# Optimization experiments

Measured on AMD Instinct MI355X. Metric: run time of the kernel, lower is better.

## Reference

```python
import jax, jax.numpy as jnp
import numpy as np

B, IN, H = 4096, 512, 1024
ALPHA, RHO = 0.001, 0.05

def setup_inputs() -> dict:
    key = jax.random.key(0)
    ks = jax.random.split(key, 9)
    inp = jax.random.normal(ks[0], (B, IN), dtype=jnp.float32)
    time = jax.random.uniform(ks[1], (B, 1), dtype=jnp.float32) * 100.0
    hx = jax.random.normal(ks[2], (B, H), dtype=jnp.float32)
    cx = jax.random.normal(ks[3], (B, H), dtype=jnp.float32)
    # params (match torch init scales loosely)
    Wxh_w = jax.random.normal(ks[4], (4 * H, IN), dtype=jnp.float32) / np.sqrt(IN)
    Wxh_b = jnp.zeros((4 * H,), dtype=jnp.float32)
    Whh_w = jax.random.normal(ks[5], (4 * H, H), dtype=jnp.float32) / np.sqrt(H)
    tau = jax.random.normal(ks[6], (H,), dtype=jnp.float32) * 0.5 + 5.0
    s = jax.random.uniform(ks[7], (H,), dtype=jnp.float32) * tau
    alpha = jnp.array([ALPHA], dtype=jnp.float32)
    rho = jnp.array([RHO], dtype=jnp.float32)
    return {"input": inp, "time": time, "hx": hx, "cx": cx,
            "Wxh_w": Wxh_w, "Wxh_b": Wxh_b, "Whh_w": Whh_w,
            "tau": tau, "s": s, "alpha": alpha, "rho": rho}

def _time_gate(time, s, tau, alpha, rho):
    # phi: [B, H] (time [B,1] broadcast against s/tau [H])
    phi = jnp.fmod(time - s, tau) / tau
    k = jnp.where(phi < rho / 2.0, 2.0 * phi / rho,
        jnp.where(phi < rho, 2.0 - 2.0 * phi / rho, alpha * phi))
    # computed under torch.no_grad() in the original
    return jax.lax.stop_gradient(k)

def reference(input, time, hx, cx, Wxh_w, Wxh_b, Whh_w, tau, s, alpha, rho):
    gates = input @ Wxh_w.T + Wxh_b + hx @ Whh_w.T  # [B, 4H]
    i, f, g, o = jnp.split(gates, 4, axis=1)
    k = _time_gate(time, s, tau, alpha, rho)
    ft = jax.nn.sigmoid(f + 1.0 - k)
    it = jax.nn.sigmoid(i) * k
    gt = jnp.tanh(g) * k
    ot = jax.nn.sigmoid(o) * k
    cy = ft * cx + it * gt
    hy = ot * jnp.tanh(cy)
    return (hy, cy)
```

## Files before the change

kernel.cpp:

```cpp
#include <hip/hip_runtime.h>

#define AS1 __attribute__((address_space(1)))
#define AS3 __attribute__((address_space(3)))

typedef _Float16 half_t;
typedef __attribute__((ext_vector_type(8))) _Float16 f16x8;
typedef __attribute__((ext_vector_type(4))) float f32x4;

static constexpr int Bsz = 4096;
static constexpr int INs = 512;
static constexpr int Hs  = 1024;
static constexpr int BM  = 128;
static constexpr int BH  = 32;
static constexpr int BK  = 64;
static constexpr int NIT = INs / BK + Hs / BK;

static constexpr size_t XN  = (size_t)Bsz * INs;
static constexpr size_t HXN = (size_t)Bsz * Hs;
static constexpr size_t WXN = (size_t)4 * Hs * INs;
static constexpr size_t WHN = (size_t)4 * Hs * Hs;
static constexpr size_t OFF_X  = 0;
static constexpr size_t OFF_HX = XN;
static constexpr size_t OFF_WX = XN + HXN;
static constexpr size_t OFF_WH = XN + HXN + WXN;
static constexpr size_t TOT    = XN + HXN + WXN + WHN;
static constexpr size_t KN     = (size_t)Bsz * Hs;

__device__ __forceinline__ float sigm(float x) {
  return 1.0f / (1.0f + __expf(-x));
}
__device__ __forceinline__ float tanh_fast(float x) {
  const float e = __expf(2.0f * x);
  return 1.0f - 2.0f / (e + 1.0f);
}

__global__ __launch_bounds__(256)
void cvt_kernel(const float* __restrict__ x, const float* __restrict__ hx,
                const float* __restrict__ wx, const float* __restrict__ wh,
                const float* __restrict__ timep, const float* __restrict__ sp,
                const float* __restrict__ taup, const float* __restrict__ alphap,
                const float* __restrict__ rhop,
                half_t* __restrict__ ws, float* __restrict__ kout) {
  const size_t cid = (size_t)blockIdx.x * 256 + threadIdx.x;
  if (cid < TOT / 8) {
    const size_t e = cid * 8;
    const float* src; size_t off;
    if (e < OFF_HX)      { src = x;  off = e - OFF_X; }
    else if (e < OFF_WX) { src = hx; off = e - OFF_HX; }
    else if (e < OFF_WH) { src = wx; off = e - OFF_WX; }
    else                 { src = wh; off = e - OFF_WH; }
    const f32x4 a = *(const f32x4*)(src + off);
    const f32x4 b = *(const f32x4*)(src + off + 4);
    f16x8 o;
    o[0]=(half_t)a[0]; o[1]=(half_t)a[1]; o[2]=(half_t)a[2]; o[3]=(half_t)a[3];
    o[4]=(half_t)b[0]; o[5]=(half_t)b[1]; o[6]=(half_t)b[2]; o[7]=(half_t)b[3];
    *(f16x8*)(ws + e) = o;
  } else {
    const size_t e2 = (cid - TOT / 8) * 8;
    const int b = (int)(e2 >> 10);
    const int h = (int)(e2 & 1023);
    const float tv = timep[b];
    const float alphav = alphap[0];
    const float rhov   = rhop[0];
    const float rh     = 0.5f * rhov;
    const f32x4 s0 = *(const f32x4*)(sp + h),   s1 = *(const f32x4*)(sp + h + 4);
    const f32x4 t0 = *(const f32x4*)(taup + h), t1 = *(const f32x4*)(taup + h + 4);
    f32x4 k0, k1;
    #pragma unroll
    for (int j = 0; j < 8; ++j) {
      const float sv   = j < 4 ? s0[j] : s1[j - 4];
      const float tauv = j < 4 ? t0[j] : t1[j - 4];
      const float phi = fmodf(tv - sv, tauv) / tauv;
      float kv;
      if (phi < rh)        kv = (2.0f * phi) / rhov;
      else if (phi < rhov) kv = 2.0f - (2.0f * phi) / rhov;
      else                 kv = alphav * phi;
      if (j < 4) k0[j] = kv; else k1[j - 4] = kv;
    }
    *(f32x4*)(kout + e2) = k0;
    *(f32x4*)(kout + e2 + 4) = k1;
  }
}

__global__ __launch_bounds__(256, 4)
void plstm_gemm(const half_t* __restrict__ xin,
                const half_t* __restrict__ hxp,
                const float* __restrict__ cxp,
                const half_t* __restrict__ wxh,
                const float* __restrict__ biasp,
                const half_t* __restrict__ whh,
                const float* __restrict__ kp,
                float* __restrict__ outp)
{
  __shared__ half_t As[BM * BK];
  __shared__ half_t Bs[BM * BK];

  const int tid  = threadIdx.x;
  const int w    = tid >> 6;
  const int lane = tid & 63;
  const int l15  = lane & 15;
  const int grp  = lane >> 4;
  const int wr   = w >> 1;
  const int wc   = w & 1;

  const int m0 = blockIdx.x * BM;
  const int h0 = blockIdx.y * BH;

  f32x4 acc[4][4] = {};

  const int ldr = tid >> 3;
  const int ldc = tid & 7;

  for (int it = 0; it < NIT; ++it) {
    const bool p1 = it >= INs / BK;
    const half_t* Ap = p1 ? hxp : xin;
    const half_t* Wp = p1 ? whh : wxh;
    const int Ka = p1 ? Hs : INs;
    const int k0 = (p1 ? (it - INs / BK) : it) * BK;
    #pragma unroll
    for (int i = 0; i < 4; ++i) {
      const int e    = i * 32 + ldr;
      const int gc8  = ldc ^ (e & 7);
      const int wrow = ((e >> 4) & 3) * Hs + h0 + ((e >> 6) << 4) + (e & 15);
      const half_t* ga = Ap + (size_t)(m0 + e) * Ka + (k0 + gc8 * 8);
      __builtin_amdgcn_global_load_lds((AS1 void*)ga,
                                       (AS3 void*)(As + (e * 8 + ldc) * 8), 16, 0, 0);
      const half_t* gw = Wp + (size_t)wrow * Ka + (k0 + gc8 * 8);
      __builtin_amdgcn_global_load_lds((AS1 void*)gw,
                                       (AS3 void*)(Bs + (e * 8 + ldc) * 8), 16, 0, 0);
    }
    __syncthreads();

    #pragma unroll
    for (int kk = 0; kk < 2; ++kk) {
      const int c8x = kk * 4 + grp;
      f16x8 af[4], bfr[4];
      #pragma unroll
      for (int mt = 0; mt < 4; ++mt) {
        const int e = wr * 64 + mt * 16 + l15;
        af[mt] = *(const f16x8*)(As + (e * 8 + (c8x ^ (l15 & 7))) * 8);
      }
      #pragma unroll
      for (int nt = 0; nt < 4; ++nt) {
        const int e = wc * 64 + nt * 16 + l15;
        bfr[nt] = *(const f16x8*)(Bs + (e * 8 + (c8x ^ (l15 & 7))) * 8);
      }
      #pragma unroll
      for (int mt = 0; mt < 4; ++mt)
        #pragma unroll
        for (int nt = 0; nt < 4; ++nt)
          acc[mt][nt] = __builtin_amdgcn_mfma_f32_16x16x32_f16(
              af[mt], bfr[nt], acc[mt][nt], 0, 0, 0);
    }
    __syncthreads();
  }

  const int h = h0 + wc * 16 + l15;
  const float bi  = biasp[h];
  const float bfv = biasp[Hs + h];
  const float bg  = biasp[2 * Hs + h];
  const float bo  = biasp[3 * Hs + h];

  #pragma unroll
  for (int mt = 0; mt < 4; ++mt) {
    #pragma unroll
    for (int r = 0; r < 4; ++r) {
      const int brow = m0 + wr * 64 + mt * 16 + grp * 4 + r;
      const float kv = kp[(size_t)brow * Hs + h];
      const float iv = acc[mt][0][r] + bi;
      const float fv = acc[mt][1][r] + bfv;
      const float gv = acc[mt][2][r] + bg;
      const float ov = acc[mt][3][r] + bo;

      const float cxv = cxp[(size_t)brow * Hs + h];
      const float ft = sigm(fv + 1.0f - kv);
      const float it2 = sigm(iv) * kv;
      const float gt = tanh_fast(gv) * kv;
      const float ot = sigm(ov) * kv;
      const float cy = ft * cxv + it2 * gt;
      const float hy = ot * tanh_fast(cy);

      outp[(size_t)brow * Hs + h] = hy;
      outp[(size_t)Bsz * Hs + (size_t)brow * Hs + h] = cy;
    }
  }
}

__global__ __launch_bounds__(256, 3)
void plstm_gemm_f32(const float* __restrict__ xin, const float* __restrict__ timep,
                    const float* __restrict__ hxp, const float* __restrict__ cxp,
                    const float* __restrict__ wxh, const float* __restrict__ biasp,
                    const float* __restrict__ whh, const float* __restrict__ taup,
                    const float* __restrict__ sp, const float* __restrict__ alphap,
                    const float* __restrict__ rhop, float* __restrict__ outp)
{
  __shared__ half_t As[BM * BK];
  __shared__ half_t Bs[BM * BK];

  const int tid  = threadIdx.x;
  const int w    = tid >> 6;
  const int lane = tid & 63;
  const int l15  = lane & 15;
  const int grp  = lane >> 4;
  const int wr   = w >> 1;
  const int wc   = w & 1;

  const int m0 = blockIdx.x * BM;
  const int h0 = blockIdx.y * BH;

  f32x4 acc[4][4] = {};
  const int ldr = tid >> 3;
  const int ldc = tid & 7;

  for (int it = 0; it < NIT; ++it) {
    const bool p1 = it >= INs / BK;
    const float* Ap = p1 ? hxp : xin;
    const float* Wp = p1 ? whh : wxh;
    const int Ka = p1 ? Hs : INs;
    const int k0 = (p1 ? (it - INs / BK) : it) * BK;
    #pragma unroll
    for (int i = 0; i < 4; ++i) {
      const int e    = i * 32 + ldr;
      const int gc8  = ldc ^ (e & 7);
      const int wrow = ((e >> 4) & 3) * Hs + h0 + ((e >> 6) << 4) + (e & 15);
      const float* ga = Ap + (size_t)(m0 + e) * Ka + (k0 + gc8 * 8);
      const f32x4 a0 = *(const f32x4*)ga, a1 = *(const f32x4*)(ga + 4);
      f16x8 pa;
      pa[0]=(half_t)a0[0]; pa[1]=(half_t)a0[1]; pa[2]=(half_t)a0[2]; pa[3]=(half_t)a0[3];
      pa[4]=(half_t)a1[0]; pa[5]=(half_t)a1[1]; pa[6]=(half_t)a1[2]; pa[7]=(half_t)a1[3];
      *(f16x8*)(As + (e * 8 + ldc) * 8) = pa;
      const float* gw = Wp + (size_t)wrow * Ka + (k0 + gc8 * 8);
      const f32x4 b0 = *(const f32x4*)gw, b1 = *(const f32x4*)(gw + 4);
      f16x8 pb;
      pb[0]=(half_t)b0[0]; pb[1]=(half_t)b0[1]; pb[2]=(half_t)b0[2]; pb[3]=(half_t)b0[3];
      pb[4]=(half_t)b1[0]; pb[5]=(half_t)b1[1]; pb[6]=(half_t)b1[2]; pb[7]=(half_t)b1[3];
      *(f16x8*)(Bs + (e * 8 + ldc) * 8) = pb;
    }
    __syncthreads();
    #pragma unroll
    for (int kk = 0; kk < 2; ++kk) {
      const int c8x = kk * 4 + grp;
      f16x8 af[4], bfr[4];
      #pragma unroll
      for (int mt = 0; mt < 4; ++mt) {
        const int e = wr * 64 + mt * 16 + l15;
        af[mt] = *(const f16x8*)(As + (e * 8 + (c8x ^ (l15 & 7))) * 8);
      }
      #pragma unroll
      for (int nt = 0; nt < 4; ++nt) {
        const int e = wc * 64 + nt * 16 + l15;
        bfr[nt] = *(const f16x8*)(Bs + (e * 8 + (c8x ^ (l15 & 7))) * 8);
      }
      #pragma unroll
      for (int mt = 0; mt < 4; ++mt)
        #pragma unroll
        for (int nt = 0; nt < 4; ++nt)
          acc[mt][nt] = __builtin_amdgcn_mfma_f32_16x16x32_f16(
              af[mt], bfr[nt], acc[mt][nt], 0, 0, 0);
    }
    __syncthreads();
  }

  const int h = h0 + wc * 16 + l15;
  const float bi  = biasp[h];
  const float bfv = biasp[Hs + h];
  const float bg  = biasp[2 * Hs + h];
  const float bo  = biasp[3 * Hs + h];
  const float sv = sp[h], tauv = taup[h];
  const float alphav = alphap[0], rhov = rhop[0], rh = 0.5f * rhov;

  #pragma unroll
  for (int mt = 0; mt < 4; ++mt) {
    #pragma unroll
    for (int r = 0; r < 4; ++r) {
      const int brow = m0 + wr * 64 + mt * 16 + grp * 4 + r;
      const float tv = timep[brow];
      const float phi = fmodf(tv - sv, tauv) / tauv;
      float kv;
      if (phi < rh)        kv = (2.0f * phi) / rhov;
      else if (phi < rhov) kv = 2.0f - (2.0f * phi) / rhov;
      else                 kv = alphav * phi;
      const float iv = acc[mt][0][r] + bi;
      const float fv = acc[mt][1][r] + bfv;
      const float gv = acc[mt][2][r] + bg;
      const float ov = acc[mt][3][r] + bo;
      const float cxv = cxp[(size_t)brow * Hs + h];
      const float ft = sigm(fv + 1.0f - kv);
      const float it2 = sigm(iv) * kv;
      const float gt = tanh_fast(gv) * kv;
      const float ot = sigm(ov) * kv;
      const float cy = ft * cxv + it2 * gt;
      const float hy = ot * tanh_fast(cy);
      outp[(size_t)brow * Hs + h] = hy;
      outp[(size_t)Bsz * Hs + (size_t)brow * Hs + h] = cy;
    }
  }
}

extern "C" void kernel_launch(void* const* d_in, const int* in_sizes, int n_in,
                              void* d_out, int out_size, void* d_ws, size_t ws_size,
                              hipStream_t stream) {
  (void)in_sizes; (void)n_in; (void)out_size;
  const float* xin   = (const float*)d_in[0];
  const float* timep = (const float*)d_in[1];
  const float* hxp   = (const float*)d_in[2];
  const float* cxp   = (const float*)d_in[3];
  const float* wxh   = (const float*)d_in[4];
  const float* biasp = (const float*)d_in[5];
  const float* whh   = (const float*)d_in[6];
  const float* taup  = (const float*)d_in[7];
  const float* sp    = (const float*)d_in[8];
  const float* alphap= (const float*)d_in[9];
  const float* rhop  = (const float*)d_in[10];
  float* outp = (float*)d_out;

  dim3 grid(Bsz / BM, Hs / BH);
  const bool wsK = ws_size >= TOT * sizeof(half_t) + KN * sizeof(float);

  if (wsK) {
    half_t* ws = (half_t*)d_ws;
    float* kout = (float*)(ws + TOT);
    const int nchunk = (int)(TOT / 8 + KN / 8);
    cvt_kernel<<<nchunk / 256, 256, 0, stream>>>(xin, hxp, wxh, whh,
                                                 timep, sp, taup, alphap, rhop,
                                                 ws, kout);
    plstm_gemm<<<grid, 256, 0, stream>>>(
        ws + OFF_X, ws + OFF_HX, cxp, ws + OFF_WX, biasp, ws + OFF_WH,
        kout, outp);
  } else {
    plstm_gemm_f32<<<grid, 256, 0, stream>>>(
        xin, timep, hxp, cxp, wxh, biasp, whh,
        taup, sp, alphap, rhop, outp);
  }
}
```

Measured before the change: 198.5 us.

## Fuse time gate into GEMM epilogue, double-buffer A tile, load weights directly

```diff
diff --git a/kernel.cpp b/kernel.cpp
--- a/kernel.cpp
+++ b/kernel.cpp
@@ -24,7 +24,6 @@
 static constexpr size_t OFF_WX = XN + HXN;
 static constexpr size_t OFF_WH = XN + HXN + WXN;
 static constexpr size_t TOT    = XN + HXN + WXN + WHN;
-static constexpr size_t KN     = (size_t)Bsz * Hs;
 
 __device__ __forceinline__ float sigm(float x) {
   return 1.0f / (1.0f + __expf(-x));
@@ -37,49 +36,20 @@
 __global__ __launch_bounds__(256)
 void cvt_kernel(const float* __restrict__ x, const float* __restrict__ hx,
                 const float* __restrict__ wx, const float* __restrict__ wh,
-                const float* __restrict__ timep, const float* __restrict__ sp,
-                const float* __restrict__ taup, const float* __restrict__ alphap,
-                const float* __restrict__ rhop,
-                half_t* __restrict__ ws, float* __restrict__ kout) {
+                half_t* __restrict__ ws) {
   const size_t cid = (size_t)blockIdx.x * 256 + threadIdx.x;
-  if (cid < TOT / 8) {
-    const size_t e = cid * 8;
-    const float* src; size_t off;
-    if (e < OFF_HX)      { src = x;  off = e - OFF_X; }
-    else if (e < OFF_WX) { src = hx; off = e - OFF_HX; }
-    else if (e < OFF_WH) { src = wx; off = e - OFF_WX; }
-    else                 { src = wh; off = e - OFF_WH; }
-    const f32x4 a = *(const f32x4*)(src + off);
-    const f32x4 b = *(const f32x4*)(src + off + 4);
-    f16x8 o;
-    o[0]=(half_t)a[0]; o[1]=(half_t)a[1]; o[2]=(half_t)a[2]; o[3]=(half_t)a[3];
-    o[4]=(half_t)b[0]; o[5]=(half_t)b[1]; o[6]=(half_t)b[2]; o[7]=(half_t)b[3];
-    *(f16x8*)(ws + e) = o;
-  } else {
-    const size_t e2 = (cid - TOT / 8) * 8;
-    const int b = (int)(e2 >> 10);
-    const int h = (int)(e2 & 1023);
-    const float tv = timep[b];
-    const float alphav = alphap[0];
-    const float rhov   = rhop[0];
-    const float rh     = 0.5f * rhov;
-    const f32x4 s0 = *(const f32x4*)(sp + h),   s1 = *(const f32x4*)(sp + h + 4);
-    const f32x4 t0 = *(const f32x4*)(taup + h), t1 = *(const f32x4*)(taup + h + 4);
-    f32x4 k0, k1;
-    #pragma unroll
-    for (int j = 0; j < 8; ++j) {
-      const float sv   = j < 4 ? s0[j] : s1[j - 4];
-      const float tauv = j < 4 ? t0[j] : t1[j - 4];
-      const float phi = fmodf(tv - sv, tauv) / tauv;
-      float kv;
-      if (phi < rh)        kv = (2.0f * phi) / rhov;
-      else if (phi < rhov) kv = 2.0f - (2.0f * phi) / rhov;
-      else                 kv = alphav * phi;
-      if (j < 4) k0[j] = kv; else k1[j - 4] = kv;
-    }
-    *(f32x4*)(kout + e2) = k0;
-    *(f32x4*)(kout + e2 + 4) = k1;
-  }
+  const size_t e = cid * 8;
+  const float* src; size_t off;
+  if (e < OFF_HX)      { src = x;  off = e - OFF_X; }
+  else if (e < OFF_WX) { src = hx; off = e - OFF_HX; }
+  else if (e < OFF_WH) { src = wx; off = e - OFF_WX; }
+  else                 { src = wh; off = e - OFF_WH; }
+  const f32x4 a = *(const f32x4*)(src + off);
+  const f32x4 b = *(const f32x4*)(src + off + 4);
+  f16x8 o;
+  o[0]=(half_t)a[0]; o[1]=(half_t)a[1]; o[2]=(half_t)a[2]; o[3]=(half_t)a[3];
+  o[4]=(half_t)b[0]; o[5]=(half_t)b[1]; o[6]=(half_t)b[2]; o[7]=(half_t)b[3];
+  *(f16x8*)(ws + e) = o;
 }
 
 __global__ __launch_bounds__(256, 4)
@@ -89,11 +59,14 @@
                 const half_t* __restrict__ wxh,
                 const float* __restrict__ biasp,
                 const half_t* __restrict__ whh,
-                const float* __restrict__ kp,
+                const float* __restrict__ timep,
+                const float* __restrict__ taup,
+                const float* __restrict__ sp,
+                const float* __restrict__ alphap,
+                const float* __restrict__ rhop,
                 float* __restrict__ outp)
 {
-  __shared__ half_t As[BM * BK];
-  __shared__ half_t Bs[BM * BK];
+  __shared__ half_t As[2][BM * BK];
 
   const int tid  = threadIdx.x;
   const int w    = tid >> 6;
@@ -105,73 +78,91 @@
 
   const int m0 = blockIdx.x * BM;
   const int h0 = blockIdx.y * BH;
+  const int hcol = h0 + wc * 16 + l15;
 
   f32x4 acc[4][4] = {};
 
   const int ldr = tid >> 3;
   const int ldc = tid & 7;
 
+  auto stageA = [&](int it, int buf) {
+    const bool p1 = it >= INs / BK;
+    const half_t* Ap = p1 ? hxp : xin;
+    const int Ka = p1 ? Hs : INs;
+    const int k0 = (p1 ? (it - INs / BK) : it) * BK;
+    #pragma unroll
+    for (int i = 0; i < 4; ++i) {
+      const int e   = i * 32 + ldr;
+      const int gc8 = ldc ^ (e & 7);
+      const half_t* ga = Ap + (size_t)(m0 + e) * Ka + (k0 + gc8 * 8);
+      __builtin_amdgcn_global_load_lds((AS1 void*)ga,
+                                       (AS3 void*)(&As[buf][(e * 8 + ldc) * 8]), 16, 0, 0);
+    }
+  };
+
+  stageA(0, 0);
+  __syncthreads();
+
   for (int it = 0; it < NIT; ++it) {
     const bool p1 = it >= INs / BK;
-    const half_t* Ap = p1 ? hxp : xin;
     const half_t* Wp = p1 ? whh : wxh;
     const int Ka = p1 ? Hs : INs;
     const int k0 = (p1 ? (it - INs / BK) : it) * BK;
-    #pragma unroll
-    for (int i = 0; i < 4; ++i) {
-      const int e    = i * 32 + ldr;
-      const int gc8  = ldc ^ (e & 7);
-      const int wrow = ((e >> 4) & 3) * Hs + h0 + ((e >> 6) << 4) + (e & 15);
-      const half_t* ga = Ap + (size_t)(m0 + e) * Ka + (k0 + gc8 * 8);
-      __builtin_amdgcn_global_load_lds((AS1 void*)ga,
-                                       (AS3 void*)(As + (e * 8 + ldc) * 8), 16, 0, 0);
-      const half_t* gw = Wp + (size_t)wrow * Ka + (k0 + gc8 * 8);
-      __builtin_amdgcn_global_load_lds((AS1 void*)gw,
-                                       (AS3 void*)(Bs + (e * 8 + ldc) * 8), 16, 0, 0);
-    }
-    __syncthreads();
-
+
+    if (it + 1 < NIT) stageA(it + 1, (it + 1) & 1);
+
+    f16x8 bfr[2][4];
+    #pragma unroll
+    for (int kk = 0; kk < 2; ++kk)
+      #pragma unroll
+      for (int nt = 0; nt < 4; ++nt)
+        bfr[kk][nt] = *(const f16x8*)(Wp + (size_t)(nt * Hs + hcol) * Ka
+                                      + k0 + (kk * 4 + grp) * 8);
+
+    const half_t* as = As[it & 1];
     #pragma unroll
     for (int kk = 0; kk < 2; ++kk) {
       const int c8x = kk * 4 + grp;
-      f16x8 af[4], bfr[4];
+      f16x8 af[4];
       #pragma unroll
       for (int mt = 0; mt < 4; ++mt) {
         const int e = wr * 64 + mt * 16 + l15;
-        af[mt] = *(const f16x8*)(As + (e * 8 + (c8x ^ (l15 & 7))) * 8);
-      }
-      #pragma unroll
-      for (int nt = 0; nt < 4; ++nt) {
-        const int e = wc * 64 + nt * 16 + l15;
-        bfr[nt] = *(const f16x8*)(Bs + (e * 8 + (c8x ^ (l15 & 7))) * 8);
+        af[mt] = *(const f16x8*)(as + (e * 8 + (c8x ^ (l15 & 7))) * 8);
       }
       #pragma unroll
       for (int mt = 0; mt < 4; ++mt)
         #pragma unroll
         for (int nt = 0; nt < 4; ++nt)
           acc[mt][nt] = __builtin_amdgcn_mfma_f32_16x16x32_f16(
-              af[mt], bfr[nt], acc[mt][nt], 0, 0, 0);
+              af[mt], bfr[kk][nt], acc[mt][nt], 0, 0, 0);
     }
     __syncthreads();
   }
 
-  const int h = h0 + wc * 16 + l15;
+  const int h = hcol;
   const float bi  = biasp[h];
   const float bfv = biasp[Hs + h];
   const float bg  = biasp[2 * Hs + h];
   const float bo  = biasp[3 * Hs + h];
+  const float sv = sp[h], tauv = taup[h];
+  const float alphav = alphap[0], rhov = rhop[0], rh = 0.5f * rhov;
 
   #pragma unroll
   for (int mt = 0; mt < 4; ++mt) {
     #pragma unroll
     for (int r = 0; r < 4; ++r) {
       const int brow = m0 + wr * 64 + mt * 16 + grp * 4 + r;
-      const float kv = kp[(size_t)brow * Hs + h];
+      const float tv = timep[brow];
+      const float phi = fmodf(tv - sv, tauv) / tauv;
+      float kv;
+      if (phi < rh)        kv = (2.0f * phi) / rhov;
+      else if (phi < rhov) kv = 2.0f - (2.0f * phi) / rhov;
+      else                 kv = alphav * phi;
+
       const float iv = acc[mt][0][r] + bi;
       const float fv = acc[mt][1][r] + bfv;
       const float gv = acc[mt][2][r] + bg;
       const float ov = acc[mt][3][r] + bo;
-
       const float cxv = cxp[(size_t)brow * Hs + h];
       const float ft = sigm(fv + 1.0f - kv);
       const float it2 = sigm(iv) * kv;
@@ -315,18 +306,12 @@
   float* outp = (float*)d_out;
 
   dim3 grid(Bsz / BM, Hs / BH);
-  const bool wsK = ws_size >= TOT * sizeof(half_t) + KN * sizeof(float);
-
-  if (wsK) {
+  if (ws_size >= TOT * sizeof(half_t)) {
     half_t* ws = (half_t*)d_ws;
-    float* kout = (float*)(ws + TOT);
-    const int nchunk = (int)(TOT / 8 + KN / 8);
-    cvt_kernel<<<nchunk / 256, 256, 0, stream>>>(xin, hxp, wxh, whh,
-                                                 timep, sp, taup, alphap, rhop,
-                                                 ws, kout);
+    cvt_kernel<<<(int)(TOT / 8 / 256), 256, 0, stream>>>(xin, hxp, wxh, whh, ws);
     plstm_gemm<<<grid, 256, 0, stream>>>(
         ws + OFF_X, ws + OFF_HX, cxp, ws + OFF_WX, biasp, ws + OFF_WH,
-        kout, outp);
+        timep, taup, sp, alphap, rhop, outp);
   } else {
     plstm_gemm_f32<<<grid, 256, 0, stream>>>(
         xin, timep, hxp, cxp, wxh, biasp, whh,
```

After: 238.8 us. 20.3% more time.
